# Optimization experiments

Measured on AMD Instinct MI355X. Metric: run time of the kernel, lower is better.

Reference implementation:

```python
import jax, jax.numpy as jnp
import numpy as np


def batch_pairwise_dist(x, y):
    # x: (B, Nx, 3), y: (B, Ny, 3) -> P: (B, Nx, Ny) squared euclidean dists
    xx = jnp.sum(x * x, axis=-1)                      # (B, Nx)
    yy = jnp.sum(y * y, axis=-1)                      # (B, Ny)
    zz = jnp.einsum('bnd,bmd->bnm', x, y)             # (B, Nx, Ny)
    return xx[:, :, None] + yy[:, None, :] - 2.0 * zz


def huber(x, c):
    return jnp.where(x < c, 0.5 * x * x, c * x - 0.5 * c * c)


def global_align_loss(preds, gts, c):
    # preds, gts: (B, N, 3) point sets; faithful to GlobalAlignLoss.forward
    P = batch_pairwise_dist(gts, preds)               # (B, Ngt, Npred)
    loss_1 = jnp.sum(huber(jnp.min(P, axis=1), c))
    loss_2 = jnp.sum(huber(jnp.min(P, axis=2), c))
    return loss_1 + loss_2


def setup_inputs() -> dict:
    key = jax.random.key(0)
    ks = jax.random.split(key, 8)
    B, KP, K, N = 4, 512, 32, 4096
    return {
        'src_keypoints': jax.random.normal(ks[0], (B, 3, KP), dtype=jnp.float32),
        'tgt_keypoints': jax.random.normal(ks[1], (B, 3, KP), dtype=jnp.float32),
        'rotation_ab': jax.random.normal(ks[2], (B, 3, 3), dtype=jnp.float32),
        'translation_ab': jax.random.normal(ks[3], (B, 3), dtype=jnp.float32),
        'src_keypoints_knn': jax.random.normal(ks[4], (B, 3, KP, K), dtype=jnp.float32),
        'tgt_keypoints_knn': jax.random.normal(ks[5], (B, 3, KP, K), dtype=jnp.float32),
        'k': K,
        'src_transformed': jax.random.normal(ks[6], (B, 3, N), dtype=jnp.float32),
        'tgt': jax.random.normal(ks[7], (B, 3, N), dtype=jnp.float32),
    }


def reference(src_keypoints, tgt_keypoints, rotation_ab, translation_ab,
              src_keypoints_knn, tgt_keypoints_knn, k, src_transformed, tgt):
    margin = 0.01  # loss_margin from init
    # Global alignment loss on full clouds (points last -> points first)
    gal = global_align_loss(jnp.transpose(src_transformed, (0, 2, 1)),
                            jnp.transpose(tgt, (0, 2, 1)), margin)
    # se3.transform: p' = R @ p + t, applied to keypoints (B, 3, KP)
    transformed_srckps = jnp.einsum('bij,bjn->bin', rotation_ab, src_keypoints) \
        + translation_ab[:, :, None]
    keypoints_loss = jnp.sum((transformed_srckps - tgt_keypoints) ** 2)
    knn_consensus_loss = jnp.sum((src_keypoints_knn - tgt_keypoints_knn) ** 2)
    neighborhood_consensus_loss = knn_consensus_loss / k + keypoints_loss
    return (neighborhood_consensus_loss, gal)
```

## Files before the change

### kernel.cpp

```cpp
#include <hip/hip_runtime.h>

#define NPTS 4096
#define NB   4
#define KP   512
#define HUBER_C 0.01f
#define HALF_PTS (NB * NPTS)
#define TOT_PTS  (2 * NB * NPTS)
#define GAL_BLOCKS 1024
#define OSTRIPE 128
#define QPT 4

typedef float v2f __attribute__((ext_vector_type(2)));




__device__ inline void wave_reduce_add_to(float v, float* target) {
    #pragma unroll
    for (int off = 32; off; off >>= 1) v += __shfl_down(v, off, 64);
    if ((threadIdx.x & 63) == 0) atomicAdd(target, v);
}

__device__ inline float huber_f(float x) {
    return (x < HUBER_C) ? 0.5f * x * x
                         : fmaf(HUBER_C, x, -0.5f * HUBER_C * HUBER_C);
}

__device__ inline v2f splat2(float s) { v2f r; r.x = s; r.y = s; return r; }


__global__ __launch_bounds__(256) void prep_kernel(
    const float* __restrict__ srcT, const float* __restrict__ tgtT,
    float4* __restrict__ pts4, unsigned* __restrict__ minarr,
    unsigned* __restrict__ ctrl)
{
    int i = blockIdx.x * 256 + threadIdx.x;
    int b = i >> 12, j = i & (NPTS - 1);
    const float* s = srcT + b * 3 * NPTS;
    const float* t = tgtT + b * 3 * NPTS;
    float sx = s[j], sy = s[NPTS + j], sz = s[2 * NPTS + j];
    float tx = t[j], ty = t[NPTS + j], tz = t[2 * NPTS + j];
    pts4[i]            = make_float4(sx, sy, sz, fmaf(sx, sx, fmaf(sy, sy, sz * sz)));
    pts4[HALF_PTS + i] = make_float4(tx, ty, tz, fmaf(tx, tx, fmaf(ty, ty, tz * tz)));
    minarr[i] = 0x7F800000u;
    minarr[HALF_PTS + i] = 0x7F800000u;
    if (i == 0) ctrl[0] = 0u;
}

__global__ __launch_bounds__(256) void main_kernel(
    const float4* __restrict__ pts4, unsigned* __restrict__ minarr,
    const float* __restrict__ skp, const float* __restrict__ tkp,
    const float* __restrict__ R, const float* __restrict__ T,
    const float* __restrict__ aknn, const float* __restrict__ bknn,
    const int* __restrict__ kptr, float* __restrict__ acc,
    int knn_blocks, int knn_quads)
{
    const int bid = blockIdx.x;
    const int tid = threadIdx.x;

    if (bid < GAL_BLOCKS) {
        const int oc  = bid & 31;
        const int b   = (bid >> 5) & 3;
        const int dir = (bid >> 7) & 1;
        const int qc  = bid >> 8;
        const float4* q4 = pts4 + (dir ? HALF_PTS : 0) + b * NPTS + qc * 1024;
        const float4* o4 = pts4 + (dir ? 0 : HALF_PTS) + b * NPTS + oc * OSTRIPE;

        v2f ax2[2], ay2[2], az2[2], mm2[2];
        float qw[QPT];
        #pragma unroll
        for (int p = 0; p < 2; ++p) {
            float4 Qa = q4[tid + (2 * p) * 256];
            float4 Qb = q4[tid + (2 * p + 1) * 256];
            ax2[p].x = -2.0f * Qa.x; ax2[p].y = -2.0f * Qb.x;
            ay2[p].x = -2.0f * Qa.y; ay2[p].y = -2.0f * Qb.y;
            az2[p].x = -2.0f * Qa.z; az2[p].y = -2.0f * Qb.z;
            qw[2 * p] = Qa.w; qw[2 * p + 1] = Qb.w;
            mm2[p].x = 3.0e38f; mm2[p].y = 3.0e38f;
        }

        auto step2 = [&](const float4& u, const float4& v) {
            #pragma unroll
            for (int p = 0; p < 2; ++p) {
                v2f t0 = __builtin_elementwise_fma(splat2(u.x), ax2[p],
                         __builtin_elementwise_fma(splat2(u.y), ay2[p],
                         __builtin_elementwise_fma(splat2(u.z), az2[p], splat2(u.w))));
                v2f t1 = __builtin_elementwise_fma(splat2(v.x), ax2[p],
                         __builtin_elementwise_fma(splat2(v.y), ay2[p],
                         __builtin_elementwise_fma(splat2(v.z), az2[p], splat2(v.w))));
                mm2[p].x = fminf(mm2[p].x, fminf(t0.x, t1.x));
                mm2[p].y = fminf(mm2[p].y, fminf(t0.y, t1.y));
            }
        };

        #pragma unroll 4
        for (int j = 0; j < OSTRIPE; j += 4) {
            float4 o0 = o4[j], o1 = o4[j + 1], o2 = o4[j + 2], o3 = o4[j + 3];
            step2(o0, o1);
            step2(o2, o3);
        }

        unsigned* marr = minarr + (dir * NB + b) * NPTS + qc * 1024 + tid;
        #pragma unroll
        for (int p = 0; p < 2; ++p) {
            float d0 = fmaxf(qw[2 * p]     + mm2[p].x, 0.0f);
            float d1 = fmaxf(qw[2 * p + 1] + mm2[p].y, 0.0f);
            atomicMin(&marr[(2 * p) * 256],     __float_as_uint(d0));
            atomicMin(&marr[(2 * p + 1) * 256], __float_as_uint(d1));
        }
    } else if (bid < GAL_BLOCKS + knn_blocks) {
        int i = (bid - GAL_BLOCKS) * 256 + tid;
        float sum = 0.0f;
        if (i < knn_quads) {
            float4 va = ((const float4*)aknn)[i];
            float4 vb = ((const float4*)bknn)[i];
            float dx = va.x - vb.x, dy = va.y - vb.y;
            float dz = va.z - vb.z, dw = va.w - vb.w;
            sum = fmaf(dx, dx, fmaf(dy, dy, fmaf(dz, dz, dw * dw)));
        }
        float scale = 1.0f / (float)(*kptr);
        wave_reduce_add_to(sum * scale, acc);
    } else {
        int i = (bid - GAL_BLOCKS - knn_blocks) * 256 + tid;
        int b = i >> 9;
        int n = i & (KP - 1);
        const float* r = R + b * 9;
        const float* t = T + b * 3;
        const float* s = skp + b * 3 * KP;
        const float* g = tkp + b * 3 * KP;
        float sx = s[n], sy = s[KP + n], sz = s[2 * KP + n];
        float sum = 0.0f;
        #pragma unroll
        for (int d = 0; d < 3; ++d) {
            float v = fmaf(r[d*3+0], sx, fmaf(r[d*3+1], sy, fmaf(r[d*3+2], sz, t[d])))
                      - g[d * KP + n];
            sum = fmaf(v, v, sum);
        }
        wave_reduce_add_to(sum, acc);
    }
}

__global__ __launch_bounds__(256) void finalize_kernel(
    const unsigned* __restrict__ minarr, const float* __restrict__ acc,
    float* __restrict__ out)
{
    __shared__ float red[4];
    const int tid = threadIdx.x;
    const uint4* m4 = (const uint4*)minarr;
    float sum = 0.0f;
    #pragma unroll
    for (int r = 0; r < 32; ++r) {
        uint4 v = m4[r * 256 + tid];
        sum += huber_f(__uint_as_float(v.x)) + huber_f(__uint_as_float(v.y))
             + huber_f(__uint_as_float(v.z)) + huber_f(__uint_as_float(v.w));
    }
    #pragma unroll
    for (int off = 32; off; off >>= 1) sum += __shfl_down(sum, off, 64);
    if ((tid & 63) == 0) red[tid >> 6] = sum;
    __syncthreads();
    if (tid == 0) {
        out[1] = red[0] + red[1] + red[2] + red[3];
        out[0] = *acc;
    }
}


__global__ void zero_out_kernel(float* __restrict__ out) {
    if (threadIdx.x < 2) out[threadIdx.x] = 0.0f;
}

__global__ __launch_bounds__(256) void gal_direct_kernel(
    const float* __restrict__ srcT, const float* __restrict__ tgtT,
    float* __restrict__ gal_out)
{
    const int dir = blockIdx.y >> 2;
    const int b   = blockIdx.y & 3;
    const float* qb = (dir ? tgtT : srcT) + b * 3 * NPTS;
    const float* ob = (dir ? srcT : tgtT) + b * 3 * NPTS;
    const int qi = blockIdx.x * 256 + threadIdx.x;
    const float qx = qb[qi], qy = qb[NPTS + qi], qz = qb[2 * NPTS + qi];
    float m = 3.0e38f;
    #pragma unroll 4
    for (int j = 0; j < NPTS; ++j) {
        float dx = qx - ob[j], dy = qy - ob[NPTS + j], dz = qz - ob[2 * NPTS + j];
        m = fminf(m, fmaf(dx, dx, fmaf(dy, dy, dz * dz)));
    }
    wave_reduce_add_to(huber_f(m), gal_out);
}

__global__ __launch_bounds__(256) void kp_kernel(
    const float* __restrict__ skp, const float* __restrict__ tkp,
    const float* __restrict__ R, const float* __restrict__ T,
    float* __restrict__ acc)
{
    int i = blockIdx.x * 256 + threadIdx.x;
    int b = i >> 9, n = i & (KP - 1);
    const float* r = R + b * 9;
    const float* t = T + b * 3;
    const float* s = skp + b * 3 * KP;
    const float* g = tkp + b * 3 * KP;
    float sx = s[n], sy = s[KP + n], sz = s[2 * KP + n];
    float sum = 0.0f;
    #pragma unroll
    for (int d = 0; d < 3; ++d) {
        float v = fmaf(r[d*3+0], sx, fmaf(r[d*3+1], sy, fmaf(r[d*3+2], sz, t[d])))
                  - g[d * KP + n];
        sum = fmaf(v, v, sum);
    }
    wave_reduce_add_to(sum, acc);
}

__global__ __launch_bounds__(256) void knn_kernel(
    const float* __restrict__ a, const float* __restrict__ b,
    const int* __restrict__ kptr, float* __restrict__ acc, int quads)
{
    int i = blockIdx.x * 256 + threadIdx.x;
    float sum = 0.0f;
    if (i < quads) {
        float4 va = ((const float4*)a)[i];
        float4 vb = ((const float4*)b)[i];
        float dx = va.x - vb.x, dy = va.y - vb.y;
        float dz = va.z - vb.z, dw = va.w - vb.w;
        sum = fmaf(dx, dx, fmaf(dy, dy, fmaf(dz, dz, dw * dw)));
    }
    float scale = 1.0f / (float)(*kptr);
    wave_reduce_add_to(sum * scale, acc);
}


extern "C" void kernel_launch(void* const* d_in, const int* in_sizes, int n_in,
                              void* d_out, int out_size, void* d_ws, size_t ws_size,
                              hipStream_t stream) {
    const float* skp  = (const float*)d_in[0];
    const float* tkp  = (const float*)d_in[1];
    const float* R    = (const float*)d_in[2];
    const float* T    = (const float*)d_in[3];
    const float* aknn = (const float*)d_in[4];
    const float* bknn = (const float*)d_in[5];
    const int*   kptr = (const int*)d_in[6];
    const float* srcT = (const float*)d_in[7];
    const float* tgtT = (const float*)d_in[8];
    float* out = (float*)d_out;

    const int knn_quads  = in_sizes[4] / 4;
    const int knn_blocks = (knn_quads + 255) / 256;
    const int kp_blocks  = (NB * KP + 255) / 256;

    const size_t pts_bytes = (size_t)TOT_PTS * 16;
    const size_t min_bytes = (size_t)TOT_PTS * 4;
    const size_t ws_need   = pts_bytes + min_bytes + 64;
    if (ws_size >= ws_need) {
        float4*   pts4   = (float4*)d_ws;
        unsigned* minarr = (unsigned*)((char*)d_ws + pts_bytes);
        unsigned* ctrl   = (unsigned*)((char*)d_ws + pts_bytes + min_bytes);
        float*    acc    = (float*)&ctrl[0];
        prep_kernel<<<HALF_PTS / 256, 256, 0, stream>>>(srcT, tgtT, pts4, minarr, ctrl);
        main_kernel<<<GAL_BLOCKS + knn_blocks + kp_blocks, 256, 0, stream>>>(
            pts4, minarr, skp, tkp, R, T, aknn, bknn, kptr, acc,
            knn_blocks, knn_quads);
        finalize_kernel<<<1, 256, 0, stream>>>(minarr, acc, out);
    } else {
        zero_out_kernel<<<1, 64, 0, stream>>>(out);
        gal_direct_kernel<<<dim3(NPTS / 256, 2 * NB), 256, 0, stream>>>(srcT, tgtT, out + 1);
        kp_kernel<<<kp_blocks, 256, 0, stream>>>(skp, tkp, R, T, out);
        knn_kernel<<<knn_blocks, 256, 0, stream>>>(aknn, bknn, kptr, out, knn_quads);
    }
}
```

Before: 93.29 us.

## Fuse point packing into main kernel with LDS-staged opponent stripes

Removes the separate packing pass that wrote float4 points with squared norms to workspace. The main kernel now reads the SoA inputs directly, computes norms on the fly and stages each 64-point opponent stripe in shared memory. Stripes are halved, so the GAL block count doubles to 2048, and launch bounds request 6 waves per SIMD. The init kernel only fills the min array, and finalize uses 1024 threads. This trades redundant norm computation, a block barrier and twice as many atomicMin calls for less global traffic and one less full pass over the points.

```diff
diff --git a/kernel.cpp b/kernel.cpp
--- a/kernel.cpp
+++ b/kernel.cpp
@@ -6,9 +6,11 @@
 #define HUBER_C 0.01f
 #define HALF_PTS (NB * NPTS)
 #define TOT_PTS  (2 * NB * NPTS)
-#define GAL_BLOCKS 1024
-#define OSTRIPE 128
-#define QPT 4
+#define OSTRIPE 64
+#define QCHUNK  1024
+#define NOC (NPTS / OSTRIPE)
+#define NQC (NPTS / QCHUNK)
+#define GAL_BLOCKS (2 * NB * NQC * NOC)
 
 typedef float v2f __attribute__((ext_vector_type(2)));
 
@@ -29,55 +31,58 @@
 __device__ inline v2f splat2(float s) { v2f r; r.x = s; r.y = s; return r; }
 
 
-__global__ __launch_bounds__(256) void prep_kernel(
+__global__ __launch_bounds__(256) void init_kernel(
+    uint4* __restrict__ minarr4, unsigned* __restrict__ ctrl)
+{
+    int i = blockIdx.x * 256 + threadIdx.x;
+    minarr4[i] = make_uint4(0x7F800000u, 0x7F800000u, 0x7F800000u, 0x7F800000u);
+    if (i == 0) ctrl[0] = 0u;
+}
+
+__global__ __launch_bounds__(256, 6) void main_kernel(
     const float* __restrict__ srcT, const float* __restrict__ tgtT,
-    float4* __restrict__ pts4, unsigned* __restrict__ minarr,
-    unsigned* __restrict__ ctrl)
-{
-    int i = blockIdx.x * 256 + threadIdx.x;
-    int b = i >> 12, j = i & (NPTS - 1);
-    const float* s = srcT + b * 3 * NPTS;
-    const float* t = tgtT + b * 3 * NPTS;
-    float sx = s[j], sy = s[NPTS + j], sz = s[2 * NPTS + j];
-    float tx = t[j], ty = t[NPTS + j], tz = t[2 * NPTS + j];
-    pts4[i]            = make_float4(sx, sy, sz, fmaf(sx, sx, fmaf(sy, sy, sz * sz)));
-    pts4[HALF_PTS + i] = make_float4(tx, ty, tz, fmaf(tx, tx, fmaf(ty, ty, tz * tz)));
-    minarr[i] = 0x7F800000u;
-    minarr[HALF_PTS + i] = 0x7F800000u;
-    if (i == 0) ctrl[0] = 0u;
-}
-
-__global__ __launch_bounds__(256) void main_kernel(
-    const float4* __restrict__ pts4, unsigned* __restrict__ minarr,
+    unsigned* __restrict__ minarr,
     const float* __restrict__ skp, const float* __restrict__ tkp,
     const float* __restrict__ R, const float* __restrict__ T,
     const float* __restrict__ aknn, const float* __restrict__ bknn,
     const int* __restrict__ kptr, float* __restrict__ acc,
     int knn_blocks, int knn_quads)
 {
+    __shared__ float4 olds[OSTRIPE];
     const int bid = blockIdx.x;
     const int tid = threadIdx.x;
 
     if (bid < GAL_BLOCKS) {
-        const int oc  = bid & 31;
-        const int b   = (bid >> 5) & 3;
-        const int dir = (bid >> 7) & 1;
-        const int qc  = bid >> 8;
-        const float4* q4 = pts4 + (dir ? HALF_PTS : 0) + b * NPTS + qc * 1024;
-        const float4* o4 = pts4 + (dir ? 0 : HALF_PTS) + b * NPTS + oc * OSTRIPE;
+        const int oc  = bid & (NOC - 1);
+        const int b   = (bid >> 6) & 3;
+        const int dir = (bid >> 8) & 1;
+        const int qc  = bid >> 9;
+        const float* qb = (dir ? tgtT : srcT) + b * 3 * NPTS;
+        const float* ob = (dir ? srcT : tgtT) + b * 3 * NPTS;
+
+        if (tid < OSTRIPE) {
+            int oi = oc * OSTRIPE + tid;
+            float ox = ob[oi], oy = ob[NPTS + oi], oz = ob[2 * NPTS + oi];
+            olds[tid] = make_float4(ox, oy, oz,
+                                    fmaf(ox, ox, fmaf(oy, oy, oz * oz)));
+        }
 
         v2f ax2[2], ay2[2], az2[2], mm2[2];
-        float qw[QPT];
+        float qw[4];
         #pragma unroll
         for (int p = 0; p < 2; ++p) {
-            float4 Qa = q4[tid + (2 * p) * 256];
-            float4 Qb = q4[tid + (2 * p + 1) * 256];
-            ax2[p].x = -2.0f * Qa.x; ax2[p].y = -2.0f * Qb.x;
-            ay2[p].x = -2.0f * Qa.y; ay2[p].y = -2.0f * Qb.y;
-            az2[p].x = -2.0f * Qa.z; az2[p].y = -2.0f * Qb.z;
-            qw[2 * p] = Qa.w; qw[2 * p + 1] = Qb.w;
+            int ia = qc * QCHUNK + (2 * p) * 256 + tid;
+            int ib = ia + 256;
+            float Ax = qb[ia], Ay = qb[NPTS + ia], Az = qb[2 * NPTS + ia];
+            float Bx = qb[ib], By = qb[NPTS + ib], Bz = qb[2 * NPTS + ib];
+            ax2[p].x = -2.0f * Ax; ax2[p].y = -2.0f * Bx;
+            ay2[p].x = -2.0f * Ay; ay2[p].y = -2.0f * By;
+            az2[p].x = -2.0f * Az; az2[p].y = -2.0f * Bz;
+            qw[2 * p]     = fmaf(Ax, Ax, fmaf(Ay, Ay, Az * Az));
+            qw[2 * p + 1] = fmaf(Bx, Bx, fmaf(By, By, Bz * Bz));
             mm2[p].x = 3.0e38f; mm2[p].y = 3.0e38f;
         }
+        __syncthreads();
 
         auto step2 = [&](const float4& u, const float4& v) {
             #pragma unroll
@@ -95,12 +100,13 @@
 
         #pragma unroll 4
         for (int j = 0; j < OSTRIPE; j += 4) {
-            float4 o0 = o4[j], o1 = o4[j + 1], o2 = o4[j + 2], o3 = o4[j + 3];
+            float4 o0 = olds[j], o1 = olds[j + 1];
+            float4 o2 = olds[j + 2], o3 = olds[j + 3];
             step2(o0, o1);
             step2(o2, o3);
         }
 
-        unsigned* marr = minarr + (dir * NB + b) * NPTS + qc * 1024 + tid;
+        unsigned* marr = minarr + (dir * NB + b) * NPTS + qc * QCHUNK + tid;
         #pragma unroll
         for (int p = 0; p < 2; ++p) {
             float d0 = fmaxf(qw[2 * p]     + mm2[p].x, 0.0f);
@@ -140,17 +146,17 @@
     }
 }
 
-__global__ __launch_bounds__(256) void finalize_kernel(
+__global__ __launch_bounds__(1024) void finalize_kernel(
     const unsigned* __restrict__ minarr, const float* __restrict__ acc,
     float* __restrict__ out)
 {
-    __shared__ float red[4];
+    __shared__ float red[16];
     const int tid = threadIdx.x;
     const uint4* m4 = (const uint4*)minarr;
     float sum = 0.0f;
     #pragma unroll
-    for (int r = 0; r < 32; ++r) {
-        uint4 v = m4[r * 256 + tid];
+    for (int r = 0; r < 8; ++r) {
+        uint4 v = m4[r * 1024 + tid];
         sum += huber_f(__uint_as_float(v.x)) + huber_f(__uint_as_float(v.y))
              + huber_f(__uint_as_float(v.z)) + huber_f(__uint_as_float(v.w));
     }
@@ -159,7 +165,10 @@
     if ((tid & 63) == 0) red[tid >> 6] = sum;
     __syncthreads();
     if (tid == 0) {
-        out[1] = red[0] + red[1] + red[2] + red[3];
+        float s = 0.0f;
+        #pragma unroll
+        for (int i = 0; i < 16; ++i) s += red[i];
+        out[1] = s;
         out[0] = *acc;
     }
 }
@@ -246,19 +255,17 @@
     const int knn_blocks = (knn_quads + 255) / 256;
     const int kp_blocks  = (NB * KP + 255) / 256;
 
-    const size_t pts_bytes = (size_t)TOT_PTS * 16;
     const size_t min_bytes = (size_t)TOT_PTS * 4;
-    const size_t ws_need   = pts_bytes + min_bytes + 64;
+    const size_t ws_need   = min_bytes + 64;
     if (ws_size >= ws_need) {
-        float4*   pts4   = (float4*)d_ws;
-        unsigned* minarr = (unsigned*)((char*)d_ws + pts_bytes);
-        unsigned* ctrl   = (unsigned*)((char*)d_ws + pts_bytes + min_bytes);
+        unsigned* minarr = (unsigned*)d_ws;
+        unsigned* ctrl   = (unsigned*)((char*)d_ws + min_bytes);
         float*    acc    = (float*)&ctrl[0];
-        prep_kernel<<<HALF_PTS / 256, 256, 0, stream>>>(srcT, tgtT, pts4, minarr, ctrl);
+        init_kernel<<<TOT_PTS / 4 / 256, 256, 0, stream>>>((uint4*)minarr, ctrl);
         main_kernel<<<GAL_BLOCKS + knn_blocks + kp_blocks, 256, 0, stream>>>(
-            pts4, minarr, skp, tkp, R, T, aknn, bknn, kptr, acc,
+            srcT, tgtT, minarr, skp, tkp, R, T, aknn, bknn, kptr, acc,
             knn_blocks, knn_quads);
-        finalize_kernel<<<1, 256, 0, stream>>>(minarr, acc, out);
+        finalize_kernel<<<1, 1024, 0, stream>>>(minarr, acc, out);
     } else {
         zero_out_kernel<<<1, 64, 0, stream>>>(out);
         gal_direct_kernel<<<dim3(NPTS / 256, 2 * NB), 256, 0, stream>>>(srcT, tgtT, out + 1);
```

New measurement: 91.74 us. Within noise of the previous version (-1.7%).

## Stage full opposing cloud in LDS per block and drop atomicMin min-array pass

Applied to the files above, without the earlier changes.

Each GAL block now covers 128 query points against the entire opposing cloud of 4096 points. It loads that cloud from the raw SoA input into LDS, with squared norms computed on the fly. Two half-block groups each scan half the cloud, their minima are combined through shared memory, and Huber is applied in-kernel. This removes the prep kernel, the global min array with its atomicMin traffic, and the finalize kernel, and uses block-level reductions with one atomicAdd per block. The cost is 64KB of LDS per block, which limits occupancy, and the cloud is reloaded and recomputed by every block.

```diff
diff --git a/kernel.cpp b/kernel.cpp
--- a/kernel.cpp
+++ b/kernel.cpp
@@ -4,22 +4,14 @@
 #define NB   4
 #define KP   512
 #define HUBER_C 0.01f
-#define HALF_PTS (NB * NPTS)
-#define TOT_PTS  (2 * NB * NPTS)
-#define GAL_BLOCKS 1024
-#define OSTRIPE 128
-#define QPT 4
+#define QCHUNK 128
+#define NQC (NPTS / QCHUNK)
+#define GAL_BLOCKS (2 * NB * NQC)
+#define NPK (NPTS / 2)
 
 typedef float v2f __attribute__((ext_vector_type(2)));
 
 
-
-
-__device__ inline void wave_reduce_add_to(float v, float* target) {
-    #pragma unroll
-    for (int off = 32; off; off >>= 1) v += __shfl_down(v, off, 64);
-    if ((threadIdx.x & 63) == 0) atomicAdd(target, v);
-}
 
 __device__ inline float huber_f(float x) {
     return (x < HUBER_C) ? 0.5f * x * x
@@ -29,99 +21,93 @@
 __device__ inline v2f splat2(float s) { v2f r; r.x = s; r.y = s; return r; }
 
 
-__global__ __launch_bounds__(256) void prep_kernel(
-    const float* __restrict__ srcT, const float* __restrict__ tgtT,
-    float4* __restrict__ pts4, unsigned* __restrict__ minarr,
-    unsigned* __restrict__ ctrl)
-{
-    int i = blockIdx.x * 256 + threadIdx.x;
-    int b = i >> 12, j = i & (NPTS - 1);
-    const float* s = srcT + b * 3 * NPTS;
-    const float* t = tgtT + b * 3 * NPTS;
-    float sx = s[j], sy = s[NPTS + j], sz = s[2 * NPTS + j];
-    float tx = t[j], ty = t[NPTS + j], tz = t[2 * NPTS + j];
-    pts4[i]            = make_float4(sx, sy, sz, fmaf(sx, sx, fmaf(sy, sy, sz * sz)));
-    pts4[HALF_PTS + i] = make_float4(tx, ty, tz, fmaf(tx, tx, fmaf(ty, ty, tz * tz)));
-    minarr[i] = 0x7F800000u;
-    minarr[HALF_PTS + i] = 0x7F800000u;
-    if (i == 0) ctrl[0] = 0u;
+__global__ void init_kernel(float* __restrict__ out) {
+    if (threadIdx.x < 2) out[threadIdx.x] = 0.0f;
 }
 
 __global__ __launch_bounds__(256) void main_kernel(
-    const float4* __restrict__ pts4, unsigned* __restrict__ minarr,
+    const float* __restrict__ srcT, const float* __restrict__ tgtT,
     const float* __restrict__ skp, const float* __restrict__ tkp,
     const float* __restrict__ R, const float* __restrict__ T,
     const float* __restrict__ aknn, const float* __restrict__ bknn,
-    const int* __restrict__ kptr, float* __restrict__ acc,
+    const int* __restrict__ kptr, float* __restrict__ out,
     int knn_blocks, int knn_quads)
 {
+    __shared__ float4 lds_a[NPK];
+    __shared__ float4 lds_b[NPK];
+    __shared__ float pmin[QCHUNK];
+    __shared__ float red[4];
+
     const int bid = blockIdx.x;
     const int tid = threadIdx.x;
+    const int kp_blocks = (NB * KP) / 256;
+    const int pre = knn_blocks + kp_blocks;
+    float contrib = 0.0f;
+    float* target;
 
-    if (bid < GAL_BLOCKS) {
-        const int oc  = bid & 31;
-        const int b   = (bid >> 5) & 3;
-        const int dir = (bid >> 7) & 1;
-        const int qc  = bid >> 8;
-        const float4* q4 = pts4 + (dir ? HALF_PTS : 0) + b * NPTS + qc * 1024;
-        const float4* o4 = pts4 + (dir ? 0 : HALF_PTS) + b * NPTS + oc * OSTRIPE;
+    if (bid >= pre) {
+        const int gb  = bid - pre;
+        const int qc  = gb & (NQC - 1);
+        const int b   = (gb >> 5) & 3;
+        const int dir = gb >> 7;
+        const float* qb = (dir ? tgtT : srcT) + b * 3 * NPTS;
+        const float* ob = (dir ? srcT : tgtT) + b * 3 * NPTS;
 
-        v2f ax2[2], ay2[2], az2[2], mm2[2];
-        float qw[QPT];
         #pragma unroll
-        for (int p = 0; p < 2; ++p) {
-            float4 Qa = q4[tid + (2 * p) * 256];
-            float4 Qb = q4[tid + (2 * p + 1) * 256];
-            ax2[p].x = -2.0f * Qa.x; ax2[p].y = -2.0f * Qb.x;
-            ay2[p].x = -2.0f * Qa.y; ay2[p].y = -2.0f * Qb.y;
-            az2[p].x = -2.0f * Qa.z; az2[p].y = -2.0f * Qb.z;
-            qw[2 * p] = Qa.w; qw[2 * p + 1] = Qb.w;
-            mm2[p].x = 3.0e38f; mm2[p].y = 3.0e38f;
+        for (int idx = tid; idx < NPK; idx += 256) {
+            int j = 2 * idx;
+            float2 X = *(const float2*)(ob + j);
+            float2 Y = *(const float2*)(ob + NPTS + j);
+            float2 Z = *(const float2*)(ob + 2 * NPTS + j);
+            float w0 = fmaf(X.x, X.x, fmaf(Y.x, Y.x, Z.x * Z.x));
+            float w1 = fmaf(X.y, X.y, fmaf(Y.y, Y.y, Z.y * Z.y));
+            lds_a[idx] = make_float4(X.x, X.y, Y.x, Y.y);
+            lds_b[idx] = make_float4(Z.x, Z.y, w0, w1);
         }
 
-        auto step2 = [&](const float4& u, const float4& v) {
-            #pragma unroll
-            for (int p = 0; p < 2; ++p) {
-                v2f t0 = __builtin_elementwise_fma(splat2(u.x), ax2[p],
-                         __builtin_elementwise_fma(splat2(u.y), ay2[p],
-                         __builtin_elementwise_fma(splat2(u.z), az2[p], splat2(u.w))));
-                v2f t1 = __builtin_elementwise_fma(splat2(v.x), ax2[p],
-                         __builtin_elementwise_fma(splat2(v.y), ay2[p],
-                         __builtin_elementwise_fma(splat2(v.z), az2[p], splat2(v.w))));
-                mm2[p].x = fminf(mm2[p].x, fminf(t0.x, t1.x));
-                mm2[p].y = fminf(mm2[p].y, fminf(t0.y, t1.y));
-            }
+        const int q = qc * QCHUNK + (tid & (QCHUNK - 1));
+        const float qx = qb[q], qy = qb[NPTS + q], qz = qb[2 * NPTS + q];
+        const float ax = -2.0f * qx, ay = -2.0f * qy, az = -2.0f * qz;
+        const float qw2 = fmaf(qx, qx, fmaf(qy, qy, qz * qz));
+        const int h = tid >> 7;
+        __syncthreads();
+
+        const float4* la = lds_a + h * (NPK / 2);
+        const float4* lb = lds_b + h * (NPK / 2);
+        v2f mm; mm.x = 3.0e38f; mm.y = 3.0e38f;
+        auto pack_step = [&](const float4& A, const float4& B) -> v2f {
+            v2f X, Y, Z, W;
+            X.x = A.x; X.y = A.y; Y.x = A.z; Y.y = A.w;
+            Z.x = B.x; Z.y = B.y; W.x = B.z; W.y = B.w;
+            return __builtin_elementwise_fma(X, splat2(ax),
+                   __builtin_elementwise_fma(Y, splat2(ay),
+                   __builtin_elementwise_fma(Z, splat2(az), W)));
         };
-
         #pragma unroll 4
-        for (int j = 0; j < OSTRIPE; j += 4) {
-            float4 o0 = o4[j], o1 = o4[j + 1], o2 = o4[j + 2], o3 = o4[j + 3];
-            step2(o0, o1);
-            step2(o2, o3);
+        for (int p = 0; p < NPK / 2; p += 2) {
+            v2f t0 = pack_step(la[p],     lb[p]);
+            v2f t1 = pack_step(la[p + 1], lb[p + 1]);
+            mm.x = fminf(mm.x, fminf(t0.x, t1.x));
+            mm.y = fminf(mm.y, fminf(t0.y, t1.y));
         }
-
-        unsigned* marr = minarr + (dir * NB + b) * NPTS + qc * 1024 + tid;
-        #pragma unroll
-        for (int p = 0; p < 2; ++p) {
-            float d0 = fmaxf(qw[2 * p]     + mm2[p].x, 0.0f);
-            float d1 = fmaxf(qw[2 * p + 1] + mm2[p].y, 0.0f);
-            atomicMin(&marr[(2 * p) * 256],     __float_as_uint(d0));
-            atomicMin(&marr[(2 * p + 1) * 256], __float_as_uint(d1));
-        }
-    } else if (bid < GAL_BLOCKS + knn_blocks) {
-        int i = (bid - GAL_BLOCKS) * 256 + tid;
-        float sum = 0.0f;
+        float m = fminf(mm.x, mm.y);
+        if (h) pmin[tid & (QCHUNK - 1)] = m;
+        __syncthreads();
+        if (!h) contrib = huber_f(fminf(m, pmin[tid]) + qw2);
+        target = out + 1;
+    } else if (bid < knn_blocks) {
+        int i = bid * 256 + tid;
         if (i < knn_quads) {
             float4 va = ((const float4*)aknn)[i];
             float4 vb = ((const float4*)bknn)[i];
             float dx = va.x - vb.x, dy = va.y - vb.y;
             float dz = va.z - vb.z, dw = va.w - vb.w;
-            sum = fmaf(dx, dx, fmaf(dy, dy, fmaf(dz, dz, dw * dw)));
+            contrib = fmaf(dx, dx, fmaf(dy, dy, fmaf(dz, dz, dw * dw)));
         }
-        float scale = 1.0f / (float)(*kptr);
-        wave_reduce_add_to(sum * scale, acc);
+        contrib *= 1.0f / (float)(*kptr);
+        target = out;
     } else {
-        int i = (bid - GAL_BLOCKS - knn_blocks) * 256 + tid;
+        int i = (bid - knn_blocks) * 256 + tid;
         int b = i >> 9;
         int n = i & (KP - 1);
         const float* r = R + b * 9;
@@ -129,102 +115,22 @@
         const float* s = skp + b * 3 * KP;
         const float* g = tkp + b * 3 * KP;
         float sx = s[n], sy = s[KP + n], sz = s[2 * KP + n];
-        float sum = 0.0f;
         #pragma unroll
         for (int d = 0; d < 3; ++d) {
             float v = fmaf(r[d*3+0], sx, fmaf(r[d*3+1], sy, fmaf(r[d*3+2], sz, t[d])))
                       - g[d * KP + n];
-            sum = fmaf(v, v, sum);
+            contrib = fmaf(v, v, contrib);
         }
-        wave_reduce_add_to(sum, acc);
+        target = out;
     }
-}
 
-__global__ __launch_bounds__(256) void finalize_kernel(
-    const unsigned* __restrict__ minarr, const float* __restrict__ acc,
-    float* __restrict__ out)
-{
-    __shared__ float red[4];
-    const int tid = threadIdx.x;
-    const uint4* m4 = (const uint4*)minarr;
-    float sum = 0.0f;
+    float v = contrib;
     #pragma unroll
-    for (int r = 0; r < 32; ++r) {
-        uint4 v = m4[r * 256 + tid];
-        sum += huber_f(__uint_as_float(v.x)) + huber_f(__uint_as_float(v.y))
-             + huber_f(__uint_as_float(v.z)) + huber_f(__uint_as_float(v.w));
-    }
-    #pragma unroll
-    for (int off = 32; off; off >>= 1) sum += __shfl_down(sum, off, 64);
-    if ((tid & 63) == 0) red[tid >> 6] = sum;
+    for (int off = 32; off; off >>= 1) v += __shfl_down(v, off, 64);
+    if ((tid & 63) == 0) red[tid >> 6] = v;
     __syncthreads();
-    if (tid == 0) {
-        out[1] = red[0] + red[1] + red[2] + red[3];
-        out[0] = *acc;
-    }
-}
-
-
-__global__ void zero_out_kernel(float* __restrict__ out) {
-    if (threadIdx.x < 2) out[threadIdx.x] = 0.0f;
-}
-
-__global__ __launch_bounds__(256) void gal_direct_kernel(
-    const float* __restrict__ srcT, const float* __restrict__ tgtT,
-    float* __restrict__ gal_out)
-{
-    const int dir = blockIdx.y >> 2;
-    const int b   = blockIdx.y & 3;
-    const float* qb = (dir ? tgtT : srcT) + b * 3 * NPTS;
-    const float* ob = (dir ? srcT : tgtT) + b * 3 * NPTS;
-    const int qi = blockIdx.x * 256 + threadIdx.x;
-    const float qx = qb[qi], qy = qb[NPTS + qi], qz = qb[2 * NPTS + qi];
-    float m = 3.0e38f;
-    #pragma unroll 4
-    for (int j = 0; j < NPTS; ++j) {
-        float dx = qx - ob[j], dy = qy - ob[NPTS + j], dz = qz - ob[2 * NPTS + j];
-        m = fminf(m, fmaf(dx, dx, fmaf(dy, dy, dz * dz)));
-    }
-    wave_reduce_add_to(huber_f(m), gal_out);
-}
-
-__global__ __launch_bounds__(256) void kp_kernel(
-    const float* __restrict__ skp, const float* __restrict__ tkp,
-    const float* __restrict__ R, const float* __restrict__ T,
-    float* __restrict__ acc)
-{
-    int i = blockIdx.x * 256 + threadIdx.x;
-    int b = i >> 9, n = i & (KP - 1);
-    const float* r = R + b * 9;
-    const float* t = T + b * 3;
-    const float* s = skp + b * 3 * KP;
-    const float* g = tkp + b * 3 * KP;
-    float sx = s[n], sy = s[KP + n], sz = s[2 * KP + n];
-    float sum = 0.0f;
-    #pragma unroll
-    for (int d = 0; d < 3; ++d) {
-        float v = fmaf(r[d*3+0], sx, fmaf(r[d*3+1], sy, fmaf(r[d*3+2], sz, t[d])))
-                  - g[d * KP + n];
-        sum = fmaf(v, v, sum);
-    }
-    wave_reduce_add_to(sum, acc);
-}
-
-__global__ __launch_bounds__(256) void knn_kernel(
-    const float* __restrict__ a, const float* __restrict__ b,
-    const int* __restrict__ kptr, float* __restrict__ acc, int quads)
-{
-    int i = blockIdx.x * 256 + threadIdx.x;
-    float sum = 0.0f;
-    if (i < quads) {
-        float4 va = ((const float4*)a)[i];
-        float4 vb = ((const float4*)b)[i];
-        float dx = va.x - vb.x, dy = va.y - vb.y;
-        float dz = va.z - vb.z, dw = va.w - vb.w;
-        sum = fmaf(dx, dx, fmaf(dy, dy, fmaf(dz, dz, dw * dw)));
-    }
-    float scale = 1.0f / (float)(*kptr);
-    wave_reduce_add_to(sum * scale, acc);
+    if (tid == 0)
+        atomicAdd(target, red[0] + red[1] + red[2] + red[3]);
 }
 
 
@@ -245,24 +151,10 @@
     const int knn_quads  = in_sizes[4] / 4;
     const int knn_blocks = (knn_quads + 255) / 256;
     const int kp_blocks  = (NB * KP + 255) / 256;
+    const int total      = knn_blocks + kp_blocks + GAL_BLOCKS;
 
-    const size_t pts_bytes = (size_t)TOT_PTS * 16;
-    const size_t min_bytes = (size_t)TOT_PTS * 4;
-    const size_t ws_need   = pts_bytes + min_bytes + 64;
-    if (ws_size >= ws_need) {
-        float4*   pts4   = (float4*)d_ws;
-        unsigned* minarr = (unsigned*)((char*)d_ws + pts_bytes);
-        unsigned* ctrl   = (unsigned*)((char*)d_ws + pts_bytes + min_bytes);
-        float*    acc    = (float*)&ctrl[0];
-        prep_kernel<<<HALF_PTS / 256, 256, 0, stream>>>(srcT, tgtT, pts4, minarr, ctrl);
-        main_kernel<<<GAL_BLOCKS + knn_blocks + kp_blocks, 256, 0, stream>>>(
-            pts4, minarr, skp, tkp, R, T, aknn, bknn, kptr, acc,
-            knn_blocks, knn_quads);
-        finalize_kernel<<<1, 256, 0, stream>>>(minarr, acc, out);
-    } else {
-        zero_out_kernel<<<1, 64, 0, stream>>>(out);
-        gal_direct_kernel<<<dim3(NPTS / 256, 2 * NB), 256, 0, stream>>>(srcT, tgtT, out + 1);
-        kp_kernel<<<kp_blocks, 256, 0, stream>>>(skp, tkp, R, T, out);
-        knn_kernel<<<knn_blocks, 256, 0, stream>>>(aknn, bknn, kptr, out, knn_quads);
-    }
+    init_kernel<<<1, 64, 0, stream>>>(out);
+    main_kernel<<<total, 256, 0, stream>>>(
+        srcT, tgtT, skp, tkp, R, T, aknn, bknn, kptr, out,
+        knn_blocks, knn_quads);
 }
```

Result: no change. 95.04 us (+1.9%).
